# Kernel optimization log

Hardware: AMD Instinct MI355X
Metric: run time of the kernel (lower is better)

## Reference

```python
import jax, jax.numpy as jnp
import numpy as np

B, I, O, D, H = 64, 1152, 32, 8, 16
NUM_ITERS = 3


def squash(s, axis=-1, eps=1e-08):
    sq = jnp.sum(s * s, axis=axis, keepdims=True)
    return (sq / (1.0 + sq)) * s / jnp.sqrt(sq + eps)


def setup_inputs() -> dict:
    key = jax.random.key(0)
    k1, k2 = jax.random.split(key)
    u = jax.random.normal(k1, (B, I, D), dtype=jnp.float32)
    weight = jax.random.normal(k2, (I, O, D, H), dtype=jnp.float32) * 0.1
    return {"u": u, "weight": weight}


def reference(u, weight):
    # u_hat: [b, i, o, h]
    u_hat = jnp.einsum('bid,iodh->bioh', u, weight)
    logits = jnp.zeros(u_hat.shape[:3], dtype=u_hat.dtype)

    def body(logits, _):
        coupling = jax.nn.softmax(logits, axis=-1)        # [b,i,o]
        s = jnp.einsum('bio,bioh->boh', coupling, u_hat)  # [b,o,h]
        v = squash(s)                                     # [b,o,h]
        logits = logits + jnp.einsum('boh,bioh->bio', v, u_hat)
        return logits, v

    _, vs = jax.lax.scan(body, logits, None, length=NUM_ITERS)
    return vs[-1]
```

## Files before the change

kernel.cpp:

```cpp
#include <hip/hip_runtime.h>

#define BB 64
#define II 1152
#define OO 32
#define DD 8
#define HH 16
#define BOH (BB * OO * HH)
#define WTILE (OO * DD * HH)

#define IC   9
#define NIC  128
#define NBB  16
#define NBG  4
#define NJB  4

#define NRNG 32
#define ICR  (II / NRNG)

typedef _Float16 half8 __attribute__((ext_vector_type(8)));

#define UHN ((size_t)BB * II * OO * HH)

template<int CTRL>
__device__ __forceinline__ float dpp_add(float x)
{
    return x + __int_as_float(__builtin_amdgcn_update_dpp(
            0, __float_as_int(x), CTRL, 0xF, 0xF, false));
}

__device__ __forceinline__ float row_sum16(float x)
{
    x = dpp_add<0x121>(x);
    x = dpp_add<0x122>(x);
    x = dpp_add<0x124>(x);
    x = dpp_add<0x128>(x);
    return x;
}

__device__ __forceinline__ float add_xor32(float x)
{
#if __has_builtin(__builtin_amdgcn_permlane32_swap)
    auto r = __builtin_amdgcn_permlane32_swap(
        __float_as_uint(x), __float_as_uint(x), false, false);
    return __uint_as_float(r[0]) + __uint_as_float(r[1]);
#else
    return x + __shfl_xor(x, 32, 64);
#endif
}

__device__ __forceinline__ float add_xor16(float x)
{
#if __has_builtin(__builtin_amdgcn_permlane16_swap)
    auto r = __builtin_amdgcn_permlane16_swap(
        __float_as_uint(x), __float_as_uint(x), false, false);
    return __uint_as_float(r[0]) + __uint_as_float(r[1]);
#else
    return x + __int_as_float(__builtin_amdgcn_ds_swizzle(__float_as_int(x), 0x401F));
#endif
}

__device__ __forceinline__ int wswz(int f) { return f ^ (((f >> 7) & 31) << 2); }

__device__ __forceinline__ void stage_w_tile(const float* __restrict__ wg,
                                             float* __restrict__ wn, int tid)
{
    #pragma unroll
    for (int j = 0; j < 4; j++) {
        const int P = (tid + j * 256) * 4;
        const int g = wswz(P);
        __builtin_amdgcn_global_load_lds(
            (const __attribute__((address_space(1))) void*)(wg + g),
            (__attribute__((address_space(3))) void*)(wn + P),
            16, 0, 0);
    }
}

template<int PASS, bool ATOMIC, bool UHAT>
__global__ __launch_bounds__(256)
void pass_kernel(const float* __restrict__ u, const float* __restrict__ w,
                 const float* __restrict__ pv0, const float* __restrict__ pv1,
                 float* __restrict__ out, _Float16* __restrict__ uhat)
{
    __shared__ __align__(16) float Wsh[2][WTILE];

    const int tid   = threadIdx.x;
    const int o     = tid & 31;
    const int hh    = (tid >> 5) & 1;
    const int bq    = tid >> 6;
    const int bbase = blockIdx.y * NBB;
    const int i0    = blockIdx.x * IC;
    const int hofs  = hh * 8;
    const int swm   = o << 2;
    const int orow  = o * (DD * HH);

    stage_w_tile(w + (size_t)i0 * WTILE, Wsh[0], tid);

    float vsum[NJB][8];
    if (PASS >= 1) {
        #pragma unroll
        for (int jb = 0; jb < NJB; jb++) {
            const int b = bbase + bq * NJB + jb;
            const float* p = pv0 + ((b * OO + o) * HH + hofs);
            float4 a = *(const float4*)p;
            float4 c = *(const float4*)(p + 4);
            vsum[jb][0] = a.x; vsum[jb][1] = a.y; vsum[jb][2] = a.z; vsum[jb][3] = a.w;
            vsum[jb][4] = c.x; vsum[jb][5] = c.y; vsum[jb][6] = c.z; vsum[jb][7] = c.w;
            if (PASS == 2) {
                const float* q = pv1 + ((b * OO + o) * HH + hofs);
                float4 a2 = *(const float4*)q;
                float4 c2 = *(const float4*)(q + 4);
                vsum[jb][0] += a2.x; vsum[jb][1] += a2.y; vsum[jb][2] += a2.z; vsum[jb][3] += a2.w;
                vsum[jb][4] += c2.x; vsum[jb][5] += c2.y; vsum[jb][6] += c2.z; vsum[jb][7] += c2.w;
            }
        }
    }

    float sacc[NJB][8];
    #pragma unroll
    for (int jb = 0; jb < NJB; jb++)
        #pragma unroll
        for (int h2 = 0; h2 < 8; h2++) sacc[jb][h2] = 0.f;

    __syncthreads();

    for (int ii = 0; ii < IC; ii++) {
        const float* wcur = Wsh[ii & 1];

        if (ii + 1 < IC)
            stage_w_tile(w + (size_t)(i0 + ii + 1) * WTILE, Wsh[(ii + 1) & 1], tid);

        float us[NJB][8];
        #pragma unroll
        for (int jb = 0; jb < NJB; jb++) {
            const float* ub = u + ((size_t)(bbase + bq * NJB + jb) * II + (i0 + ii)) * DD;
            float4 a = *(const float4*)ub;
            float4 c = *(const float4*)(ub + 4);
            us[jb][0] = a.x; us[jb][1] = a.y; us[jb][2] = a.z; us[jb][3] = a.w;
            us[jb][4] = c.x; us[jb][5] = c.y; us[jb][6] = c.z; us[jb][7] = c.w;
        }

        float uh[NJB][8];
        #pragma unroll
        for (int jb = 0; jb < NJB; jb++)
            #pragma unroll
            for (int h2 = 0; h2 < 8; h2++) uh[jb][h2] = 0.f;
        #pragma unroll
        for (int d = 0; d < DD; d++) {
            const int ba  = (d * HH + hofs    ) ^ swm;
            const int bb2 = (d * HH + hofs + 4) ^ swm;
            float4 wa = *(const float4*)&wcur[orow + ba];
            float4 wb = *(const float4*)&wcur[orow + bb2];
            const float wv[8] = {wa.x, wa.y, wa.z, wa.w, wb.x, wb.y, wb.z, wb.w};
            #pragma unroll
            for (int jb = 0; jb < NJB; jb++)
                #pragma unroll
                for (int h2 = 0; h2 < 8; h2++)
                    uh[jb][h2] = fmaf(us[jb][d], wv[h2], uh[jb][h2]);
        }

        if (UHAT) {
            #pragma unroll
            for (int jb = 0; jb < NJB; jb++) {
                const int b = bbase + bq * NJB + jb;
                half8 hv;
                #pragma unroll
                for (int h2 = 0; h2 < 8; h2++) hv[h2] = (_Float16)uh[jb][h2];
                *(half8*)(uhat + (((size_t)b * II + (i0 + ii)) * OO + o) * HH + hofs) = hv;
            }
        }

        float cc[NJB];
        if (PASS == 0) {
            #pragma unroll
            for (int jb = 0; jb < NJB; jb++) cc[jb] = 1.0f / 32.0f;
        } else {
            #pragma unroll
            for (int jb = 0; jb < NJB; jb++) {
                float lg = 0.f;
                #pragma unroll
                for (int h2 = 0; h2 < 8; h2++)
                    lg = fmaf(vsum[jb][h2], uh[jb][h2], lg);
                lg = add_xor32(lg);
                const float e = __expf(lg);
                const float se = add_xor16(row_sum16(e));
                cc[jb] = __fdividef(e, se);
            }
        }

        #pragma unroll
        for (int jb = 0; jb < NJB; jb++)
            #pragma unroll
            for (int h2 = 0; h2 < 8; h2++)
                sacc[jb][h2] = fmaf(cc[jb], uh[jb][h2], sacc[jb][h2]);

        __syncthreads();
    }

    #pragma unroll
    for (int jb = 0; jb < NJB; jb++) {
        const int b = bbase + bq * NJB + jb;
        if (ATOMIC) {
            float* p = out + ((b * OO + o) * HH + hofs);
            #pragma unroll
            for (int h2 = 0; h2 < 8; h2++) atomicAdd(p + h2, sacc[jb][h2]);
        } else {
            float* p = out + ((size_t)blockIdx.x * BB + b) * (OO * HH) + o * HH + hofs;
            *(float4*)p       = make_float4(sacc[jb][0], sacc[jb][1], sacc[jb][2], sacc[jb][3]);
            *(float4*)(p + 4) = make_float4(sacc[jb][4], sacc[jb][5], sacc[jb][6], sacc[jb][7]);
        }
    }
}

template<int PASS>
__global__ __launch_bounds__(256)
void fast_pass_kernel(const _Float16* __restrict__ uhat,
                      const float* __restrict__ pv0, const float* __restrict__ pv1,
                      float* __restrict__ part)
{
    __shared__ float4 red[4][64][2];

    const int tid  = threadIdx.x;
    const int o    = tid & 31;
    const int hh   = (tid >> 5) & 1;
    const int q    = tid >> 6;
    const int b    = blockIdx.y;
    const int i0   = blockIdx.x * ICR + q * 9;
    const int hofs = hh * 8;

    half8 hv[9];
    #pragma unroll
    for (int ii = 0; ii < 9; ii++)
        hv[ii] = *(const half8*)
            (uhat + (((size_t)b * II + (i0 + ii)) * OO + o) * HH + hofs);

    float vsum[8];
    {
        const float* p = pv0 + ((b * OO + o) * HH + hofs);
        float4 a = *(const float4*)p;
        float4 c = *(const float4*)(p + 4);
        vsum[0] = a.x; vsum[1] = a.y; vsum[2] = a.z; vsum[3] = a.w;
        vsum[4] = c.x; vsum[5] = c.y; vsum[6] = c.z; vsum[7] = c.w;
        if (PASS == 2) {
            const float* qq = pv1 + ((b * OO + o) * HH + hofs);
            float4 a2 = *(const float4*)qq;
            float4 c2 = *(const float4*)(qq + 4);
            vsum[0] += a2.x; vsum[1] += a2.y; vsum[2] += a2.z; vsum[3] += a2.w;
            vsum[4] += c2.x; vsum[5] += c2.y; vsum[6] += c2.z; vsum[7] += c2.w;
        }
    }

    float sacc[8];
    #pragma unroll
    for (int h2 = 0; h2 < 8; h2++) sacc[h2] = 0.f;

    #pragma unroll
    for (int ii = 0; ii < 9; ii++) {
        float uh[8];
        #pragma unroll
        for (int h2 = 0; h2 < 8; h2++) uh[h2] = (float)hv[ii][h2];

        float lg = 0.f;
        #pragma unroll
        for (int h2 = 0; h2 < 8; h2++)
            lg = fmaf(vsum[h2], uh[h2], lg);
        lg = add_xor32(lg);
        const float e = __expf(lg);
        const float se = add_xor16(row_sum16(e));
        const float cc = __fdividef(e, se);

        #pragma unroll
        for (int h2 = 0; h2 < 8; h2++)
            sacc[h2] = fmaf(cc, uh[h2], sacc[h2]);
    }

    red[q][o + 32 * hh][0] = make_float4(sacc[0], sacc[1], sacc[2], sacc[3]);
    red[q][o + 32 * hh][1] = make_float4(sacc[4], sacc[5], sacc[6], sacc[7]);
    __syncthreads();

    if (tid < 64) {
        float4 a = red[0][tid][0], c = red[0][tid][1];
        #pragma unroll
        for (int j = 1; j < 4; j++) {
            float4 x = red[j][tid][0], y = red[j][tid][1];
            a.x += x.x; a.y += x.y; a.z += x.z; a.w += x.w;
            c.x += y.x; c.y += y.y; c.z += y.z; c.w += y.w;
        }
        float* p = part + ((size_t)blockIdx.x * BB + b) * (OO * HH)
                 + (tid & 31) * HH + (tid >> 5) * 8;
        *(float4*)p       = a;
        *(float4*)(p + 4) = c;
    }
}

template<int NCH>
__global__ __launch_bounds__(256)
void reduce_squash_wide_kernel(const float* __restrict__ part, float* __restrict__ v)
{
    const int t4l = threadIdx.x & 31;
    const int icp = threadIdx.x >> 5;
    const int t4  = blockIdx.x * 32 + t4l;

    const float4* p = (const float4*)part + t4;
    float4 acc = make_float4(0.f, 0.f, 0.f, 0.f);
    #pragma unroll
    for (int k = 0; k < NCH / 8; k++) {
        float4 x = p[(size_t)(icp * (NCH / 8) + k) * (BOH / 4)];
        acc.x += x.x; acc.y += x.y; acc.z += x.z; acc.w += x.w;
    }

    __shared__ float4 red[8][32];
    red[icp][t4l] = acc;
    __syncthreads();

    if (threadIdx.x < 32) {
        float4 a = red[0][t4l];
        #pragma unroll
        for (int j = 1; j < 8; j++) {
            float4 x = red[j][t4l];
            a.x += x.x; a.y += x.y; a.z += x.z; a.w += x.w;
        }
        float sq = a.x * a.x + a.y * a.y + a.z * a.z + a.w * a.w;
        sq = dpp_add<0xB1>(sq);
        sq = dpp_add<0x4E>(sq);
        const float scale = (sq / (1.f + sq)) * rsqrtf(sq + 1e-8f);
        a.x *= scale; a.y *= scale; a.z *= scale; a.w *= scale;
        ((float4*)v)[t4] = a;
    }
}

__global__ __launch_bounds__(256)
void squash_kernel(const float* __restrict__ s, float* __restrict__ v)
{
    const int t = blockIdx.x * blockDim.x + threadIdx.x;
    if (t >= BB * OO) return;
    const float4* sp = (const float4*)(s + t * HH);
    float4 a = sp[0], b = sp[1], c = sp[2], d = sp[3];
    float sq = a.x*a.x + a.y*a.y + a.z*a.z + a.w*a.w
             + b.x*b.x + b.y*b.y + b.z*b.z + b.w*b.w
             + c.x*c.x + c.y*c.y + c.z*c.z + c.w*c.w
             + d.x*d.x + d.y*d.y + d.z*d.z + d.w*d.w;
    const float scale = (sq / (1.f + sq)) * rsqrtf(sq + 1e-8f);
    a.x *= scale; a.y *= scale; a.z *= scale; a.w *= scale;
    b.x *= scale; b.y *= scale; b.z *= scale; b.w *= scale;
    c.x *= scale; c.y *= scale; c.z *= scale; c.w *= scale;
    d.x *= scale; d.y *= scale; d.z *= scale; d.w *= scale;
    float4* vp = (float4*)(v + t * HH);
    vp[0] = a; vp[1] = b; vp[2] = c; vp[3] = d;
}

extern "C" void kernel_launch(void* const* d_in, const int* in_sizes, int n_in,
                              void* d_out, int out_size, void* d_ws, size_t ws_size,
                              hipStream_t stream)
{
    (void)in_sizes; (void)n_in; (void)out_size;
    const float* u = (const float*)d_in[0];
    const float* w = (const float*)d_in[1];
    float* out = (float*)d_out;

    const size_t partN = (size_t)NIC * BOH;
    const size_t need  = (partN + 2 * BOH) * sizeof(float) + UHN * sizeof(_Float16);
    const dim3 blk(256);

    if (ws_size >= need) {
        float* part     = (float*)d_ws;
        float* v0       = part + partN;
        float* v1       = v0 + BOH;
        _Float16* uhat  = (_Float16*)(v1 + BOH);
        const int rblocks = BOH / 4 / 32;

        pass_kernel<0, false, true><<<dim3(NIC, NBG), blk, 0, stream>>>(
            u, w, nullptr, nullptr, part, uhat);
        reduce_squash_wide_kernel<NIC><<<rblocks, 256, 0, stream>>>(part, v0);
        fast_pass_kernel<1><<<dim3(NRNG, BB), blk, 0, stream>>>(uhat, v0, nullptr, part);
        reduce_squash_wide_kernel<NRNG><<<rblocks, 256, 0, stream>>>(part, v1);
        fast_pass_kernel<2><<<dim3(NRNG, BB), blk, 0, stream>>>(uhat, v0, v1, part);
        reduce_squash_wide_kernel<NRNG><<<rblocks, 256, 0, stream>>>(part, out);
    } else {
        float* s0 = (float*)d_ws;
        float* s1 = s0 + BOH;
        float* v0 = s1 + BOH;
        float* v1 = v0 + BOH;
        hipMemsetAsync(d_ws, 0, 2 * BOH * sizeof(float), stream);
        hipMemsetAsync(d_out, 0, BOH * sizeof(float), stream);
        const dim3 grid(NIC, NBG);
        const int sq_blocks = (BB * OO + 255) / 256;

        pass_kernel<0, true, false><<<grid, blk, 0, stream>>>(u, w, nullptr, nullptr, s0, nullptr);
        squash_kernel<<<sq_blocks, 256, 0, stream>>>(s0, v0);
        pass_kernel<1, true, false><<<grid, blk, 0, stream>>>(u, w, v0, nullptr, s1, nullptr);
        squash_kernel<<<sq_blocks, 256, 0, stream>>>(s1, v1);
        pass_kernel<2, true, false><<<grid, blk, 0, stream>>>(u, w, v0, v1, out, nullptr);
        squash_kernel<<<sq_blocks, 256, 0, stream>>>(out, out);
    }
}
```

Measured before the change: 120.7 us.

## Fuse partial-sum reduction and squash into the fast routing pass kernels

Each fast pass block now reduces the previous pass's partial sums for its batch row and applies squash itself, instead of relying on a separate reduce_squash kernel launch. This removes two kernel launches and two intermediate round trips of v through global memory. The cost is redundant work: every one of the NRNG blocks per batch re-reads and re-reduces the same partials (up to 128 chunks for pass 1), so partial-sum traffic grows. It also uses extra workspace, since separate partial buffers are kept per pass.

```diff
diff --git a/kernel.cpp b/kernel.cpp
--- a/kernel.cpp
+++ b/kernel.cpp
@@ -211,11 +211,13 @@
     }
 }
 
-template<int PASS>
+template<int PASS, int NCHP>
 __global__ __launch_bounds__(256)
-void fast_pass_kernel(const _Float16* __restrict__ uhat,
-                      const float* __restrict__ pv0, const float* __restrict__ pv1,
-                      float* __restrict__ part)
+void fast_pass2_kernel(const _Float16* __restrict__ uhat,
+                       const float* __restrict__ part_prev,
+                       const float* __restrict__ v0g,
+                       float* __restrict__ v0out,
+                       float* __restrict__ part_out)
 {
     __shared__ float4 red[4][64][2];
 
@@ -226,6 +228,7 @@
     const int b    = blockIdx.y;
     const int i0   = blockIdx.x * ICR + q * 9;
     const int hofs = hh * 8;
+    const int oh   = o + 32 * hh;
 
     half8 hv[9];
     #pragma unroll
@@ -233,20 +236,59 @@
         hv[ii] = *(const half8*)
             (uhat + (((size_t)b * II + (i0 + ii)) * OO + o) * HH + hofs);
 
+    constexpr int CPQ = NCHP / 4;
+    float pa[8];
+    #pragma unroll
+    for (int h2 = 0; h2 < 8; h2++) pa[h2] = 0.f;
+    #pragma unroll
+    for (int k = 0; k < CPQ; k++) {
+        const float* pp = part_prev
+            + ((size_t)(q * CPQ + k) * BB + b) * (OO * HH) + o * HH + hofs;
+        float4 x = *(const float4*)pp;
+        float4 y = *(const float4*)(pp + 4);
+        pa[0] += x.x; pa[1] += x.y; pa[2] += x.z; pa[3] += x.w;
+        pa[4] += y.x; pa[5] += y.y; pa[6] += y.z; pa[7] += y.w;
+    }
+    red[q][oh][0] = make_float4(pa[0], pa[1], pa[2], pa[3]);
+    red[q][oh][1] = make_float4(pa[4], pa[5], pa[6], pa[7]);
+    __syncthreads();
+
+    float s8[8];
+    {
+        float4 a = red[0][oh][0], c = red[0][oh][1];
+        #pragma unroll
+        for (int j = 1; j < 4; j++) {
+            float4 x = red[j][oh][0], y = red[j][oh][1];
+            a.x += x.x; a.y += x.y; a.z += x.z; a.w += x.w;
+            c.x += y.x; c.y += y.y; c.z += y.z; c.w += y.w;
+        }
+        s8[0] = a.x; s8[1] = a.y; s8[2] = a.z; s8[3] = a.w;
+        s8[4] = c.x; s8[5] = c.y; s8[6] = c.z; s8[7] = c.w;
+    }
+    __syncthreads();
+
+    float sq = 0.f;
+    #pragma unroll
+    for (int h2 = 0; h2 < 8; h2++) sq = fmaf(s8[h2], s8[h2], sq);
+    sq = add_xor32(sq);
+    const float scl = (sq / (1.f + sq)) * rsqrtf(sq + 1e-8f);
+
     float vsum[8];
-    {
-        const float* p = pv0 + ((b * OO + o) * HH + hofs);
+    #pragma unroll
+    for (int h2 = 0; h2 < 8; h2++) vsum[h2] = s8[h2] * scl;
+
+    if (PASS == 1) {
+        if (q == 0) {
+            float* p = v0out + ((b * OO + o) * HH + hofs);
+            *(float4*)p       = make_float4(vsum[0], vsum[1], vsum[2], vsum[3]);
+            *(float4*)(p + 4) = make_float4(vsum[4], vsum[5], vsum[6], vsum[7]);
+        }
+    } else {
+        const float* p = v0g + ((b * OO + o) * HH + hofs);
         float4 a = *(const float4*)p;
         float4 c = *(const float4*)(p + 4);
-        vsum[0] = a.x; vsum[1] = a.y; vsum[2] = a.z; vsum[3] = a.w;
-        vsum[4] = c.x; vsum[5] = c.y; vsum[6] = c.z; vsum[7] = c.w;
-        if (PASS == 2) {
-            const float* qq = pv1 + ((b * OO + o) * HH + hofs);
-            float4 a2 = *(const float4*)qq;
-            float4 c2 = *(const float4*)(qq + 4);
-            vsum[0] += a2.x; vsum[1] += a2.y; vsum[2] += a2.z; vsum[3] += a2.w;
-            vsum[4] += c2.x; vsum[5] += c2.y; vsum[6] += c2.z; vsum[7] += c2.w;
-        }
+        vsum[0] += a.x; vsum[1] += a.y; vsum[2] += a.z; vsum[3] += a.w;
+        vsum[4] += c.x; vsum[5] += c.y; vsum[6] += c.z; vsum[7] += c.w;
     }
 
     float sacc[8];
@@ -273,8 +315,8 @@
             sacc[h2] = fmaf(cc, uh[h2], sacc[h2]);
     }
 
-    red[q][o + 32 * hh][0] = make_float4(sacc[0], sacc[1], sacc[2], sacc[3]);
-    red[q][o + 32 * hh][1] = make_float4(sacc[4], sacc[5], sacc[6], sacc[7]);
+    red[q][oh][0] = make_float4(sacc[0], sacc[1], sacc[2], sacc[3]);
+    red[q][oh][1] = make_float4(sacc[4], sacc[5], sacc[6], sacc[7]);
     __syncthreads();
 
     if (tid < 64) {
@@ -285,7 +327,7 @@
             a.x += x.x; a.y += x.y; a.z += x.z; a.w += x.w;
             c.x += y.x; c.y += y.y; c.z += y.z; c.w += y.w;
         }
-        float* p = part + ((size_t)blockIdx.x * BB + b) * (OO * HH)
+        float* p = part_out + ((size_t)blockIdx.x * BB + b) * (OO * HH)
                  + (tid & 31) * HH + (tid >> 5) * 8;
         *(float4*)p       = a;
         *(float4*)(p + 4) = c;
@@ -357,24 +399,27 @@
     const float* w = (const float*)d_in[1];
     float* out = (float*)d_out;
 
-    const size_t partN = (size_t)NIC * BOH;
-    const size_t need  = (partN + 2 * BOH) * sizeof(float) + UHN * sizeof(_Float16);
+    const size_t part0N = (size_t)NIC * BOH;
+    const size_t part1N = (size_t)NRNG * BOH;
+    const size_t need   = (part0N + 2 * part1N + BOH) * sizeof(float)
+                        + UHN * sizeof(_Float16);
     const dim3 blk(256);
 
     if (ws_size >= need) {
-        float* part     = (float*)d_ws;
-        float* v0       = part + partN;
-        float* v1       = v0 + BOH;
-        _Float16* uhat  = (_Float16*)(v1 + BOH);
+        float* part0    = (float*)d_ws;
+        float* part1    = part0 + part0N;
+        float* part2    = part1 + part1N;
+        float* v0       = part2 + part1N;
+        _Float16* uhat  = (_Float16*)(v0 + BOH);
         const int rblocks = BOH / 4 / 32;
 
         pass_kernel<0, false, true><<<dim3(NIC, NBG), blk, 0, stream>>>(
-            u, w, nullptr, nullptr, part, uhat);
-        reduce_squash_wide_kernel<NIC><<<rblocks, 256, 0, stream>>>(part, v0);
-        fast_pass_kernel<1><<<dim3(NRNG, BB), blk, 0, stream>>>(uhat, v0, nullptr, part);
-        reduce_squash_wide_kernel<NRNG><<<rblocks, 256, 0, stream>>>(part, v1);
-        fast_pass_kernel<2><<<dim3(NRNG, BB), blk, 0, stream>>>(uhat, v0, v1, part);
-        reduce_squash_wide_kernel<NRNG><<<rblocks, 256, 0, stream>>>(part, out);
+            u, w, nullptr, nullptr, part0, uhat);
+        fast_pass2_kernel<1, NIC><<<dim3(NRNG, BB), blk, 0, stream>>>(
+            uhat, part0, nullptr, v0, part1);
+        fast_pass2_kernel<2, NRNG><<<dim3(NRNG, BB), blk, 0, stream>>>(
+            uhat, part1, v0, nullptr, part2);
+        reduce_squash_wide_kernel<NRNG><<<rblocks, 256, 0, stream>>>(part2, out);
     } else {
         float* s0 = (float*)d_ws;
         float* s1 = s0 + BOH;
```

Result: slower. 167.1 us (+38.4%).
